# Optimization experiments

Hardware: AMD Instinct MI355X
Metric: run time of the kernel (lower is better)

The kernel has to match this reference:

```python
import jax, jax.numpy as jnp
import numpy as np

HIDDEN = 1024
EMB = HIDDEN // 2          # embedding_dim = hidden_dim // 2
NUM_OPS = 8
BATCH = 16384


def setup_inputs() -> dict:
    key = jax.random.key(0)
    ks = jax.random.split(key, 8)
    x = jax.random.normal(ks[0], (BATCH, HIDDEN), dtype=jnp.float32)
    sampled_ops = jax.random.randint(ks[1], (BATCH,), 0, NUM_OPS, dtype=jnp.int32)
    op_emb = jax.random.normal(ks[2], (NUM_OPS, EMB), dtype=jnp.float32) * 0.02
    # per-expert 2-layer MLP params (Linear stored as [in, out] for x @ W)
    s1 = 1.0 / np.sqrt(HIDDEN + EMB)
    s2 = 1.0 / np.sqrt(HIDDEN)
    W1 = jax.random.uniform(ks[3], (NUM_OPS, HIDDEN + EMB, HIDDEN), jnp.float32, -s1, s1)
    b1 = jax.random.uniform(ks[4], (NUM_OPS, HIDDEN), jnp.float32, -s1, s1)
    W2 = jax.random.uniform(ks[5], (NUM_OPS, HIDDEN, HIDDEN), jnp.float32, -s2, s2)
    b2 = jax.random.uniform(ks[6], (NUM_OPS, HIDDEN), jnp.float32, -s2, s2)
    return {"x": x, "sampled_ops": sampled_ops, "op_emb": op_emb,
            "W1": W1, "b1": b1, "W2": W2, "b2": b2}


def reference(x, sampled_ops, op_emb, W1, b1, W2, b2):
    # gather per-token operator embedding and augment input
    emb = jnp.take(op_emb, sampled_ops, axis=0)            # [B, EMB]
    x_aug = jnp.concatenate([x, emb], axis=-1)             # [B, H+EMB]
    num_ops = W1.shape[0]
    out = jnp.zeros_like(x)
    # loop over the small fixed expert set; mask-combine per token
    for o in range(num_ops):
        h = jax.nn.relu(x_aug @ W1[o] + b1[o])             # [B, H]
        y = jax.nn.relu(h @ W2[o] + b2[o])                 # [B, H]
        mask = (sampled_ops == o)[:, None]
        out = out + jnp.where(mask, y, 0.0)
    return out
```

## Files before the change

kernel.cpp:

```cpp
#include <hip/hip_runtime.h>
#include <hip/hip_bf16.h>

#define BATCH 16384
#define HID   1024
#define EMBD  512
#define NOPS  8
#define MAXT  136
#define CNTS  16

typedef __attribute__((ext_vector_type(8))) short bf16x8;
typedef __attribute__((ext_vector_type(4))) float f32x4;

#define VMWAIT(N) asm volatile("s_waitcnt vmcnt(" #N ")" ::: "memory")
#define BARRIER_FENCED()                      \
  do {                                        \
    asm volatile("" ::: "memory");            \
    __builtin_amdgcn_s_barrier();             \
    asm volatile("" ::: "memory");            \
    __builtin_amdgcn_sched_barrier(0);        \
  } while (0)

__device__ __forceinline__ unsigned short f2bf(float f) {
  unsigned int u = __float_as_uint(f);
  u += 0x7FFF + ((u >> 16) & 1);
  return (unsigned short)(u >> 16);
}

__device__ __forceinline__ unsigned int pk2(float a, float b) {
  __hip_bfloat162 t = __float22bfloat162_rn(make_float2(a, b));
  return *(unsigned int*)(&t);
}

__device__ __forceinline__ void lds_load16(void* lds, const void* g) {
  __builtin_amdgcn_global_load_lds(
      (const __attribute__((address_space(1))) unsigned int*)g,
      (__attribute__((address_space(3))) unsigned int*)lds, 16, 0, 0);
}

__device__ __forceinline__ void decode_bid(int bid, int& g, int& nx) {
  g = 17 * (bid & 7) + (bid >> 6);
  nx = (bid >> 3) & 7;
}

__device__ __forceinline__ int decode_tile(const int* __restrict__ cnt,
                                           int g, int& rs, int& ce_cnt) {
  int e = -1, at = 0;
  rs = 0; ce_cnt = 0;
#pragma unroll
  for (int o = 0; o < NOPS; ++o) {
    int c = cnt[o * CNTS];
    int t = (c + 127) >> 7;
    if (e < 0 && g < at + t) { e = o; rs = (g - at) * 128; ce_cnt = c; }
    at += t;
  }
  return e;
}

__device__ __forceinline__ void w_prep_tile(const float* __restrict__ W,
                                            short* __restrict__ Wp,
                                            int ks, int nx, int tid) {
  int n = tid & 127, kh = tid >> 7;
  const float* src = W + (size_t)(ks * 32 + kh * 16) * 1024 + nx * 128 + n;
  float v[16];
#pragma unroll
  for (int kk = 0; kk < 16; ++kk) v[kk] = src[(size_t)kk * 1024];
  uint4 a, b;
  a.x = pk2(v[0], v[1]);  a.y = pk2(v[2], v[3]);
  a.z = pk2(v[4], v[5]);  a.w = pk2(v[6], v[7]);
  b.x = pk2(v[8], v[9]);  b.y = pk2(v[10], v[11]);
  b.z = pk2(v[12], v[13]); b.w = pk2(v[14], v[15]);
  uint4* dst = (uint4*)Wp;
  dst[(2 * kh) * 128 + n]     = a;
  dst[(2 * kh + 1) * 128 + n] = b;
}

__global__ void bucket_ce_k(const int* __restrict__ ops, int* __restrict__ cnt,
                            int* __restrict__ idx, const float* __restrict__ W1,
                            const float* __restrict__ emb,
                            const float* __restrict__ b1, float* __restrict__ ce,
                            short* __restrict__ W1p, const float* __restrict__ x,
                            unsigned int* __restrict__ xb) {
  int bid = blockIdx.x;
  int tid = threadIdx.x;
  if (bid >= 2240) {
    size_t i = ((size_t)(bid - 2240) * 256 + tid) * 16;
    const float4* src = (const float4*)(x + i);
    float4 f0 = src[0], f1 = src[1], f2v = src[2], f3 = src[3];
    uint4 p0 = make_uint4(pk2(f0.x, f0.y), pk2(f0.z, f0.w),
                          pk2(f1.x, f1.y), pk2(f1.z, f1.w));
    uint4 p1 = make_uint4(pk2(f2v.x, f2v.y), pk2(f2v.z, f2v.w),
                          pk2(f3.x, f3.y), pk2(f3.z, f3.w));
    uint4* dst = (uint4*)(xb + i / 2);
    dst[0] = p0;
    dst[1] = p1;
    return;
  }
  if (bid >= 192) {
    int b = bid - 192;
    int e = b / 256; int rr = b % 256; int nx = rr / 32, ks = rr % 32;
    w_prep_tile(W1 + (size_t)e * 1536 * 1024,
                W1p + ((size_t)(e * 8 + nx) * 32 + ks) * 4096, ks, nx, tid);
    return;
  }
  if (bid >= 64) {
    int cb = bid - 64;
    int e = cb >> 4, kp = cb & 15;
    int n = tid * 4;
    const float* Wc = W1 + (size_t)e * 1536 * 1024 + (size_t)(1024 + kp * 32) * 1024 + n;
    const float* ee = emb + e * EMBD + kp * 32;
    float4 a = make_float4(0.f, 0.f, 0.f, 0.f);
#pragma unroll
    for (int kk = 0; kk < 32; ++kk) {
      float s = ee[kk];
      float4 r = *(const float4*)(Wc + (size_t)kk * 1024);
      a.x += s * r.x; a.y += s * r.y; a.z += s * r.z; a.w += s * r.w;
    }
    if (kp == 0) {
      float4 b = *(const float4*)(b1 + e * HID + n);
      a.x += b.x; a.y += b.y; a.z += b.z; a.w += b.w;
    }
    float* d = ce + e * HID + n;
    atomicAdd(d + 0, a.x); atomicAdd(d + 1, a.y);
    atomicAdd(d + 2, a.z); atomicAdd(d + 3, a.w);
    return;
  }
  __shared__ int wcnt[4][NOPS];
  __shared__ int wbase[4][NOPS];
  int lane = tid & 63, w = tid >> 6;
  int t = bid * 256 + tid;
  int op = ops[t];
  unsigned long long msave = 0;
#pragma unroll
  for (int o = 0; o < NOPS; ++o) {
    unsigned long long mm = __ballot(op == o);
    if (op == o) msave = mm;
    if (lane == o) wcnt[w][o] = __popcll(mm);
  }
  __syncthreads();
  if (tid < NOPS) {
    int c0 = wcnt[0][tid], c1 = wcnt[1][tid], c2 = wcnt[2][tid], c3 = wcnt[3][tid];
    int base = atomicAdd(&cnt[tid * CNTS], c0 + c1 + c2 + c3);
    wbase[0][tid] = base;
    wbase[1][tid] = base + c0;
    wbase[2][tid] = base + c0 + c1;
    wbase[3][tid] = base + c0 + c1 + c2;
  }
  __syncthreads();
  int pre = __popcll(msave & ((1ull << lane) - 1ull));
  idx[op * BATCH + wbase[w][op] + pre] = t;
}

__global__ __launch_bounds__(256, 3) void gemm1_w2_k(
    const unsigned int* __restrict__ xb, const int* __restrict__ idx,
    const float* __restrict__ ce, const short* __restrict__ W1p,
    unsigned short* __restrict__ hp, const int* __restrict__ cnt,
    const float* __restrict__ W2, short* __restrict__ W2p) {
  int bid = blockIdx.x;
  int tid = threadIdx.x;
  if (bid >= 8 * MAXT) {
    int b = bid - 8 * MAXT;
    int e = b / 256; int rr = b % 256; int nx = rr / 32, ks = rr % 32;
    w_prep_tile(W2 + (size_t)e * 1024 * 1024,
                W2p + ((size_t)(e * 8 + nx) * 32 + ks) * 4096, ks, nx, tid);
    return;
  }
  int g, nx;
  decode_bid(bid, g, nx);
  int rs, ce_cnt;
  int e = decode_tile(cnt, g, rs, ce_cnt);
  if (e < 0) return;

  __shared__ __align__(16) char smem[49152];
  char* s0 = smem;
  char* s1 = smem + 16384;
  char* s2 = smem + 32768;

  int lane = tid & 63, w = tid >> 6;
  int wm = w >> 1, wn = w & 1;
  int fr = lane & 15, fq = lane >> 4;

  int r0 = w * 32 + (lane >> 2);
  int r1 = r0 + 16;
  int qs = (lane & 3) ^ ((lane >> 3) & 3);
  int pp0 = rs + r0, pp1 = rs + r1;
  int t0 = (pp0 < ce_cnt) ? idx[e * BATCH + pp0] : 0;
  int t1 = (pp1 < ce_cnt) ? idx[e * BATCH + pp1] : 0;
  const char* pa0 = (const char*)xb + (size_t)t0 * 2048 + qs * 16;
  const char* pa1 = (const char*)xb + (size_t)t1 * 2048 + qs * 16;
  const char* pb0 = (const char*)W1p + (size_t)(e * 8 + nx) * 32 * 8192
                    + w * 1024 + lane * 16;
  const char* pb1 = pb0 + 4096;

#define G1_STAGE(NB)                                                          \
  {                                                                           \
    lds_load16((NB) + w * 2048,         pa0);                                 \
    lds_load16((NB) + w * 2048 + 1024,  pa1);                                 \
    lds_load16((NB) + 8192 + w * 1024,  pb0);                                 \
    lds_load16((NB) + 12288 + w * 1024, pb1);                                 \
    pa0 += 64; pa1 += 64; pb0 += 8192; pb1 += 8192;                           \
  }

#define G1_COMP(CB)                                                           \
  {                                                                           \
    const short* lA_ = (const short*)(CB);                                    \
    const short* lB_ = (const short*)((CB) + 8192);                           \
    bf16x8 af[4], bfr[4];                                                     \
    _Pragma("unroll")                                                         \
    for (int i = 0; i < 4; ++i) af[i] = *(const bf16x8*)&lA_[fo + i * 512];   \
    _Pragma("unroll")                                                         \
    for (int j = 0; j < 4; ++j) bfr[j] = *(const bf16x8*)&lB_[bo + j * 128];  \
    _Pragma("unroll")                                                         \
    for (int i = 0; i < 4; ++i)                                               \
      _Pragma("unroll")                                                       \
      for (int j = 0; j < 4; ++j)                                             \
        acc[i][j] = __builtin_amdgcn_mfma_f32_16x16x32_bf16(af[i], bfr[j],    \
                                                            acc[i][j], 0, 0, 0); \
  }

#define G1_STEP(CB, NB)                                                       \
  {                                                                           \
    G1_STAGE(NB);                                                             \
    G1_COMP(CB);                                                              \
    VMWAIT(4);                                                                \
    BARRIER_FENCED();                                                         \
  }

  G1_STAGE(s0);
  G1_STAGE(s1);
  VMWAIT(4);
  BARRIER_FENCED();

  f32x4 acc[4][4] = {};
  int fo = (wm * 64 + fr) * 32 + (fq ^ ((fr >> 1) & 3)) * 8;
  int bo = (fq * 128 + wn * 64 + fr) * 8;

  for (int it = 0; it < 10; ++it) {
    G1_STEP(s0, s2);
    G1_STEP(s1, s0);
    G1_STEP(s2, s1);
  }
  G1_COMP(s0);
  VMWAIT(0);
  BARRIER_FENCED();
  G1_COMP(s1);

#undef G1_STEP
#undef G1_COMP
#undef G1_STAGE

  float bias[4];
#pragma unroll
  for (int j = 0; j < 4; ++j)
    bias[j] = ce[e * HID + nx * 128 + wn * 64 + j * 16 + fr];

  int lr = lane >> 2;
#pragma unroll
  for (int i = 0; i < 4; ++i) {
    __syncthreads();
#pragma unroll
    for (int j = 0; j < 4; ++j)
#pragma unroll
      for (int rg = 0; rg < 4; ++rg) {
        float v = acc[i][j][rg] + bias[j];
        v = v > 0.f ? v : 0.f;
        int row16 = fq * 4 + rg;
        int off = w * 2048 + row16 * 128 + (j * 16 + fr) * 2;
        off ^= (row16 & 1) << 6;
        *(unsigned short*)(smem + off) = f2bf(v);
      }
    __syncthreads();
    int R = wm * 64 + i * 16 + lr;
#pragma unroll
    for (int s = 0; s < 2; ++s) {
      int ch = (lane & 3) + s * 4;
      int off = w * 2048 + lr * 128 + ch * 16;
      off ^= (lr & 1) << 6;
      uint4 val = *(const uint4*)(smem + off);
      int ks2 = nx * 4 + wn * 2 + (ch >> 2);
      int kq = ch & 3;
      *(uint4*)(hp + (((size_t)(g * 32 + ks2) * 4 + kq) * 128 + R) * 8) = val;
    }
  }
}

__global__ __launch_bounds__(256, 3) void gemm2_k(
    const unsigned short* __restrict__ hp, const float* __restrict__ b2,
    const short* __restrict__ W2p, float* __restrict__ out,
    const int* __restrict__ idx, const int* __restrict__ cnt) {
  int g, nx;
  decode_bid(blockIdx.x, g, nx);
  int rs, ce_cnt;
  int e = decode_tile(cnt, g, rs, ce_cnt);
  if (e < 0) return;

  __shared__ __align__(16) char smem[49152];
  __shared__ int toks[128];
  char* s0 = smem;
  char* s1 = smem + 16384;
  char* s2 = smem + 32768;

  int tid = threadIdx.x, lane = tid & 63, w = tid >> 6;
  int wm = w >> 1, wn = w & 1;
  int fr = lane & 15, fq = lane >> 4;

  if (tid < 128) {
    int p = rs + tid;
    toks[tid] = (p < ce_cnt) ? idx[e * BATCH + p] : 0;
  }

  const char* Asrc = (const char*)hp + (size_t)g * 32 * 8192;
  const char* Bsrc = (const char*)W2p + (size_t)(e * 8 + nx) * 32 * 8192;
  const char* pA0 = Asrc + w * 1024 + lane * 16;
  const char* pA1 = pA0 + 4096;
  const char* pB0 = Bsrc + w * 1024 + lane * 16;
  const char* pB1 = pB0 + 4096;

#define G2_STAGE(NB)                                                          \
  {                                                                           \
    lds_load16((NB) + w * 1024,         pA0);                                 \
    lds_load16((NB) + 4096 + w * 1024,  pA1);                                 \
    lds_load16((NB) + 8192 + w * 1024,  pB0);                                 \
    lds_load16((NB) + 12288 + w * 1024, pB1);                                 \
    pA0 += 8192; pA1 += 8192; pB0 += 8192; pB1 += 8192;                       \
  }

#define G2_COMP(CB)                                                           \
  {                                                                           \
    const short* lA_ = (const short*)(CB);                                    \
    const short* lB_ = (const short*)((CB) + 8192);                           \
    bf16x8 af[4], bfr[4];                                                     \
    _Pragma("unroll")                                                         \
    for (int i = 0; i < 4; ++i) af[i] = *(const bf16x8*)&lA_[fo + i * 128];   \
    _Pragma("unroll")                                                         \
    for (int j = 0; j < 4; ++j) bfr[j] = *(const bf16x8*)&lB_[bo + j * 128];  \
    _Pragma("unroll")                                                         \
    for (int i = 0; i < 4; ++i)                                               \
      _Pragma("unroll")                                                       \
      for (int j = 0; j < 4; ++j)                                             \
        acc[i][j] = __builtin_amdgcn_mfma_f32_16x16x32_bf16(af[i], bfr[j],    \
                                                            acc[i][j], 0, 0, 0); \
  }

#define G2_STEP(CB, NB)                                                       \
  {                                                                           \
    G2_STAGE(NB);                                                             \
    G2_COMP(CB);                                                              \
    VMWAIT(4);                                                                \
    BARRIER_FENCED();                                                         \
  }

  G2_STAGE(s0);
  G2_STAGE(s1);
  VMWAIT(4);
  BARRIER_FENCED();

  f32x4 acc[4][4] = {};
  int fo = (fq * 128 + wm * 64 + fr) * 8;
  int bo = (fq * 128 + wn * 64 + fr) * 8;

  for (int it = 0; it < 10; ++it) {
    G2_STEP(s0, s2);
    G2_STEP(s1, s0);
    G2_STEP(s2, s1);
  }
  G2_COMP(s0);
  VMWAIT(0);
  BARRIER_FENCED();
  G2_COMP(s1);

#undef G2_STEP
#undef G2_COMP
#undef G2_STAGE

  float bias[4];
#pragma unroll
  for (int j = 0; j < 4; ++j)
    bias[j] = b2[e * HID + nx * 128 + wn * 64 + j * 16 + fr];

  int lr = lane >> 2;
#pragma unroll
  for (int i = 0; i < 4; ++i) {
    __syncthreads();
#pragma unroll
    for (int j = 0; j < 4; ++j)
#pragma unroll
      for (int rg = 0; rg < 4; ++rg) {
        float v = acc[i][j][rg] + bias[j];
        int row16 = fq * 4 + rg;
        int off = w * 4096 + row16 * 256 + (j * 16 + fr) * 4;
        off ^= (row16 & 1) << 6;
        *(float*)(smem + off) = v > 0.f ? v : 0.f;
      }
    __syncthreads();
    int R = wm * 64 + i * 16 + lr;
    if (R < ce_cnt - rs) {
      float* orow = out + (size_t)toks[R] * HID + nx * 128 + wn * 64;
#pragma unroll
      for (int s = 0; s < 4; ++s) {
        int ch = (lane & 3) + s * 4;
        int off = w * 4096 + lr * 256 + ch * 16;
        off ^= (lr & 1) << 6;
        *(float4*)(orow + ch * 4) = *(const float4*)(smem + off);
      }
    }
  }
}


extern "C" void kernel_launch(void* const* d_in, const int* in_sizes, int n_in,
                              void* d_out, int out_size, void* d_ws, size_t ws_size,
                              hipStream_t stream) {
  const float* x   = (const float*)d_in[0];
  const int*   ops = (const int*)d_in[1];
  const float* emb = (const float*)d_in[2];
  const float* W1  = (const float*)d_in[3];
  const float* b1  = (const float*)d_in[4];
  const float* W2  = (const float*)d_in[5];
  const float* b2  = (const float*)d_in[6];
  float* out = (float*)d_out;

  char* ws = (char*)d_ws;
  int* cnt  = (int*)(ws + 0);
  float* ce = (float*)(ws + 512);
  int* idx  = (int*)(ws + 36864);
  short* W1p = (short*)(ws + 561152);
  short* W2p = (short*)(ws + 17338368);
  unsigned short* hp = (unsigned short*)(ws + 34115584);
  unsigned int* xb = (unsigned int*)(ws + 69767168);

  hipMemsetAsync(ws, 0, 33280, stream);
  bucket_ce_k<<<2240 + 4096, 256, 0, stream>>>(ops, cnt, idx, W1, emb, b1, ce, W1p, x, xb);
  gemm1_w2_k<<<8 * MAXT + 2048, 256, 0, stream>>>(xb, idx, ce, W1p, hp, cnt, W2, W2p);
  gemm2_k<<<8 * MAXT, 256, 0, stream>>>(hp, b2, W2p, out, idx, cnt);
}
```

Before: 274.4 us.

## Interleave side-work blocks with main blocks in fused prep and GEMM1 launches

Block IDs in the two fused kernels are remapped so every third block does the primary work (bucketing/ce/W1 prep, or GEMM1 tiles) and the other two do the auxiliary conversions (x to bf16, or W2 packing). Previously the auxiliary blocks were appended at the end of the grid and ran only after the main blocks. Interleaving lets memory-bound conversion work run alongside compute-heavy GEMM tiles so the streams of work overlap and tail imbalance shrinks. The grids are padded to multiples of three, so some blocks exit immediately, and the GEMM tile order that was tuned for cache locality is now spread across more hardware slots.

```diff
diff --git a/kernel.cpp b/kernel.cpp
--- a/kernel.cpp
+++ b/kernel.cpp
@@ -37,9 +37,9 @@
       (__attribute__((address_space(3))) unsigned int*)lds, 16, 0, 0);
 }
 
-__device__ __forceinline__ void decode_bid(int bid, int& g, int& nx) {
-  g = 17 * (bid & 7) + (bid >> 6);
-  nx = (bid >> 3) & 7;
+__device__ __forceinline__ void decode_bid(int gb, int& g, int& nx) {
+  g = 17 * (gb & 7) + (gb >> 6);
+  nx = (gb >> 3) & 7;
 }
 
 __device__ __forceinline__ int decode_tile(const int* __restrict__ cnt,
@@ -82,8 +82,11 @@
                             unsigned int* __restrict__ xb) {
   int bid = blockIdx.x;
   int tid = threadIdx.x;
-  if (bid >= 2240) {
-    size_t i = ((size_t)(bid - 2240) * 256 + tid) * 16;
+  int q = bid / 3, r = bid - q * 3;
+  if (r != 0) {
+    int b = 2 * q + (r - 1);
+    if (b >= 4096) return;
+    size_t i = ((size_t)b * 256 + tid) * 16;
     const float4* src = (const float4*)(x + i);
     float4 f0 = src[0], f1 = src[1], f2v = src[2], f3 = src[3];
     uint4 p0 = make_uint4(pk2(f0.x, f0.y), pk2(f0.z, f0.w),
@@ -95,15 +98,15 @@
     dst[1] = p1;
     return;
   }
-  if (bid >= 192) {
-    int b = bid - 192;
+  if (q >= 192) {
+    int b = q - 192;
     int e = b / 256; int rr = b % 256; int nx = rr / 32, ks = rr % 32;
     w_prep_tile(W1 + (size_t)e * 1536 * 1024,
                 W1p + ((size_t)(e * 8 + nx) * 32 + ks) * 4096, ks, nx, tid);
     return;
   }
-  if (bid >= 64) {
-    int cb = bid - 64;
+  if (q >= 64) {
+    int cb = q - 64;
     int e = cb >> 4, kp = cb & 15;
     int n = tid * 4;
     const float* Wc = W1 + (size_t)e * 1536 * 1024 + (size_t)(1024 + kp * 32) * 1024 + n;
@@ -112,8 +115,8 @@
 #pragma unroll
     for (int kk = 0; kk < 32; ++kk) {
       float s = ee[kk];
-      float4 r = *(const float4*)(Wc + (size_t)kk * 1024);
-      a.x += s * r.x; a.y += s * r.y; a.z += s * r.z; a.w += s * r.w;
+      float4 r2 = *(const float4*)(Wc + (size_t)kk * 1024);
+      a.x += s * r2.x; a.y += s * r2.y; a.z += s * r2.z; a.w += s * r2.w;
     }
     if (kp == 0) {
       float4 b = *(const float4*)(b1 + e * HID + n);
@@ -127,7 +130,7 @@
   __shared__ int wcnt[4][NOPS];
   __shared__ int wbase[4][NOPS];
   int lane = tid & 63, w = tid >> 6;
-  int t = bid * 256 + tid;
+  int t = q * 256 + tid;
   int op = ops[t];
   unsigned long long msave = 0;
 #pragma unroll
@@ -157,15 +160,17 @@
     const float* __restrict__ W2, short* __restrict__ W2p) {
   int bid = blockIdx.x;
   int tid = threadIdx.x;
-  if (bid >= 8 * MAXT) {
-    int b = bid - 8 * MAXT;
+  int q = bid / 3, r = bid - q * 3;
+  if (r != 0) {
+    int b = 2 * q + (r - 1);
+    if (b >= 2048) return;
     int e = b / 256; int rr = b % 256; int nx = rr / 32, ks = rr % 32;
     w_prep_tile(W2 + (size_t)e * 1024 * 1024,
                 W2p + ((size_t)(e * 8 + nx) * 32 + ks) * 4096, ks, nx, tid);
     return;
   }
   int g, nx;
-  decode_bid(bid, g, nx);
+  decode_bid(q, g, nx);
   int rs, ce_cnt;
   int e = decode_tile(cnt, g, rs, ce_cnt);
   if (e < 0) return;
@@ -429,7 +434,7 @@
   unsigned int* xb = (unsigned int*)(ws + 69767168);
 
   hipMemsetAsync(ws, 0, 33280, stream);
-  bucket_ce_k<<<2240 + 4096, 256, 0, stream>>>(ops, cnt, idx, W1, emb, b1, ce, W1p, x, xb);
-  gemm1_w2_k<<<8 * MAXT + 2048, 256, 0, stream>>>(xb, idx, ce, W1p, hp, cnt, W2, W2p);
+  bucket_ce_k<<<6720, 256, 0, stream>>>(ops, cnt, idx, W1, emb, b1, ce, W1p, x, xb);
+  gemm1_w2_k<<<3264, 256, 0, stream>>>(xb, idx, ce, W1p, hp, cnt, W2, W2p);
   gemm2_k<<<8 * MAXT, 256, 0, stream>>>(hp, b2, W2p, out, idx, cnt);
 }
```

Result: no change. 278.4 us (+1.5%).

## Widen GEMM1 block tile to 128x256 to reuse A tiles across two N slices

Applied to the files above, without the earlier changes.

Each GEMM1 block now computes two adjacent 128-column output slices instead of one. Each gathered activation tile is loaded once and used for twice as many MFMAs, and the GEMM1 grid is halved. The cost is doubled accumulator registers, a larger LDS footprint of 72KB triple-buffered, and launch bounds lowered from 3 to 2 blocks per CU, so occupancy and latency hiding drop.

```diff
diff --git a/kernel.cpp b/kernel.cpp
--- a/kernel.cpp
+++ b/kernel.cpp
@@ -40,6 +40,11 @@
 __device__ __forceinline__ void decode_bid(int bid, int& g, int& nx) {
   g = 17 * (bid & 7) + (bid >> 6);
   nx = (bid >> 3) & 7;
+}
+
+__device__ __forceinline__ void decode_bid2(int gb, int& g, int& nx2) {
+  g = 17 * (gb & 7) + (gb >> 5);
+  nx2 = (gb >> 3) & 3;
 }
 
 __device__ __forceinline__ int decode_tile(const int* __restrict__ cnt,
@@ -150,30 +155,30 @@
   idx[op * BATCH + wbase[w][op] + pre] = t;
 }
 
-__global__ __launch_bounds__(256, 3) void gemm1_w2_k(
+__global__ __launch_bounds__(256, 2) void gemm1_w2_k(
     const unsigned int* __restrict__ xb, const int* __restrict__ idx,
     const float* __restrict__ ce, const short* __restrict__ W1p,
     unsigned short* __restrict__ hp, const int* __restrict__ cnt,
     const float* __restrict__ W2, short* __restrict__ W2p) {
   int bid = blockIdx.x;
   int tid = threadIdx.x;
-  if (bid >= 8 * MAXT) {
-    int b = bid - 8 * MAXT;
+  if (bid >= 544) {
+    int b = bid - 544;
     int e = b / 256; int rr = b % 256; int nx = rr / 32, ks = rr % 32;
     w_prep_tile(W2 + (size_t)e * 1024 * 1024,
                 W2p + ((size_t)(e * 8 + nx) * 32 + ks) * 4096, ks, nx, tid);
     return;
   }
-  int g, nx;
-  decode_bid(bid, g, nx);
+  int g, nx2;
+  decode_bid2(bid, g, nx2);
   int rs, ce_cnt;
   int e = decode_tile(cnt, g, rs, ce_cnt);
   if (e < 0) return;
 
-  __shared__ __align__(16) char smem[49152];
+  __shared__ __align__(16) char smem[73728];
   char* s0 = smem;
-  char* s1 = smem + 16384;
-  char* s2 = smem + 32768;
+  char* s1 = smem + 24576;
+  char* s2 = smem + 49152;
 
   int lane = tid & 63, w = tid >> 6;
   int wm = w >> 1, wn = w & 1;
@@ -187,50 +192,59 @@
   int t1 = (pp1 < ce_cnt) ? idx[e * BATCH + pp1] : 0;
   const char* pa0 = (const char*)xb + (size_t)t0 * 2048 + qs * 16;
   const char* pa1 = (const char*)xb + (size_t)t1 * 2048 + qs * 16;
-  const char* pb0 = (const char*)W1p + (size_t)(e * 8 + nx) * 32 * 8192
-                    + w * 1024 + lane * 16;
-  const char* pb1 = pb0 + 4096;
+  const char* pb00 = (const char*)W1p + (size_t)(e * 8 + nx2 * 2) * 32 * 8192
+                     + w * 1024 + lane * 16;
+  const char* pb01 = pb00 + 4096;
+  const char* pb10 = pb00 + 262144;
+  const char* pb11 = pb10 + 4096;
 
 #define G1_STAGE(NB)                                                          \
   {                                                                           \
     lds_load16((NB) + w * 2048,         pa0);                                 \
     lds_load16((NB) + w * 2048 + 1024,  pa1);                                 \
-    lds_load16((NB) + 8192 + w * 1024,  pb0);                                 \
-    lds_load16((NB) + 12288 + w * 1024, pb1);                                 \
-    pa0 += 64; pa1 += 64; pb0 += 8192; pb1 += 8192;                           \
+    lds_load16((NB) + 8192 + w * 1024,  pb00);                                \
+    lds_load16((NB) + 12288 + w * 1024, pb01);                                \
+    lds_load16((NB) + 16384 + w * 1024, pb10);                                \
+    lds_load16((NB) + 20480 + w * 1024, pb11);                                \
+    pa0 += 64; pa1 += 64;                                                     \
+    pb00 += 8192; pb01 += 8192; pb10 += 8192; pb11 += 8192;                   \
   }
 
 #define G1_COMP(CB)                                                           \
   {                                                                           \
-    const short* lA_ = (const short*)(CB);                                    \
-    const short* lB_ = (const short*)((CB) + 8192);                           \
-    bf16x8 af[4], bfr[4];                                                     \
+    const short* lA_  = (const short*)(CB);                                   \
+    const short* lB0_ = (const short*)((CB) + 8192);                          \
+    const short* lB1_ = (const short*)((CB) + 16384);                         \
+    bf16x8 af[4], bfr[8];                                                     \
     _Pragma("unroll")                                                         \
     for (int i = 0; i < 4; ++i) af[i] = *(const bf16x8*)&lA_[fo + i * 512];   \
     _Pragma("unroll")                                                         \
-    for (int j = 0; j < 4; ++j) bfr[j] = *(const bf16x8*)&lB_[bo + j * 128];  \
+    for (int j = 0; j < 4; ++j) {                                             \
+      bfr[j]     = *(const bf16x8*)&lB0_[bo + j * 128];                       \
+      bfr[4 + j] = *(const bf16x8*)&lB1_[bo + j * 128];                       \
+    }                                                                         \
     _Pragma("unroll")                                                         \
     for (int i = 0; i < 4; ++i)                                               \
       _Pragma("unroll")                                                       \
-      for (int j = 0; j < 4; ++j)                                             \
-        acc[i][j] = __builtin_amdgcn_mfma_f32_16x16x32_bf16(af[i], bfr[j],    \
-                                                            acc[i][j], 0, 0, 0); \
+      for (int jj = 0; jj < 8; ++jj)                                          \
+        acc[i][jj] = __builtin_amdgcn_mfma_f32_16x16x32_bf16(af[i], bfr[jj],  \
+                                                             acc[i][jj], 0, 0, 0); \
   }
 
 #define G1_STEP(CB, NB)                                                       \
   {                                                                           \
     G1_STAGE(NB);                                                             \
     G1_COMP(CB);                                                              \
-    VMWAIT(4);                                                                \
+    VMWAIT(6);                                                                \
     BARRIER_FENCED();                                                         \
   }
 
   G1_STAGE(s0);
   G1_STAGE(s1);
-  VMWAIT(4);
+  VMWAIT(6);
   BARRIER_FENCED();
 
-  f32x4 acc[4][4] = {};
+  f32x4 acc[4][8] = {};
   int fo = (wm * 64 + fr) * 32 + (fq ^ ((fr >> 1) & 3)) * 8;
   int bo = (fq * 128 + wn * 64 + fr) * 8;
 
@@ -248,37 +262,43 @@
 #undef G1_COMP
 #undef G1_STAGE
 
-  float bias[4];
-#pragma unroll
-  for (int j = 0; j < 4; ++j)
-    bias[j] = ce[e * HID + nx * 128 + wn * 64 + j * 16 + fr];
+  float bias[2][4];
+#pragma unroll
+  for (int h = 0; h < 2; ++h)
+#pragma unroll
+    for (int j = 0; j < 4; ++j)
+      bias[h][j] = ce[e * HID + (nx2 * 2 + h) * 128 + wn * 64 + j * 16 + fr];
 
   int lr = lane >> 2;
 #pragma unroll
-  for (int i = 0; i < 4; ++i) {
-    __syncthreads();
-#pragma unroll
-    for (int j = 0; j < 4; ++j)
-#pragma unroll
-      for (int rg = 0; rg < 4; ++rg) {
-        float v = acc[i][j][rg] + bias[j];
-        v = v > 0.f ? v : 0.f;
-        int row16 = fq * 4 + rg;
-        int off = w * 2048 + row16 * 128 + (j * 16 + fr) * 2;
-        off ^= (row16 & 1) << 6;
-        *(unsigned short*)(smem + off) = f2bf(v);
+  for (int h = 0; h < 2; ++h) {
+    int nx = nx2 * 2 + h;
+#pragma unroll
+    for (int i = 0; i < 4; ++i) {
+      __syncthreads();
+#pragma unroll
+      for (int j = 0; j < 4; ++j)
+#pragma unroll
+        for (int rg = 0; rg < 4; ++rg) {
+          float v = acc[i][h * 4 + j][rg] + bias[h][j];
+          v = v > 0.f ? v : 0.f;
+          int row16 = fq * 4 + rg;
+          int off = w * 2048 + row16 * 128 + (j * 16 + fr) * 2;
+          off ^= (row16 & 1) << 6;
+          *(unsigned short*)(smem + off) = f2bf(v);
+        }
+      __syncthreads();
+      int R = wm * 64 + i * 16 + lr;
+#pragma unroll
+      for (int s = 0; s < 2; ++s) {
+        int ch = (lane & 3) + s * 4;
+        int off = w * 2048 + lr * 128 + ch * 16;
+        off ^= (lr & 1) << 6;
+        uint4 val = *(const uint4*)(smem + off);
+        int ks2 = nx * 4 + wn * 2 + (ch >> 2);
+        int kq = ch & 3;
+        *(uint4*)(hp + (((size_t)(g * 32 + ks2) * 4 + kq) * 128 + R) * 8) = val;
       }
-    __syncthreads();
-    int R = wm * 64 + i * 16 + lr;
-#pragma unroll
-    for (int s = 0; s < 2; ++s) {
-      int ch = (lane & 3) + s * 4;
-      int off = w * 2048 + lr * 128 + ch * 16;
-      off ^= (lr & 1) << 6;
-      uint4 val = *(const uint4*)(smem + off);
-      int ks2 = nx * 4 + wn * 2 + (ch >> 2);
-      int kq = ch & 3;
-      *(uint4*)(hp + (((size_t)(g * 32 + ks2) * 4 + kq) * 128 + R) * 8) = val;
     }
   }
 }
@@ -430,6 +450,6 @@
 
   hipMemsetAsync(ws, 0, 33280, stream);
   bucket_ce_k<<<2240 + 4096, 256, 0, stream>>>(ops, cnt, idx, W1, emb, b1, ce, W1p, x, xb);
-  gemm1_w2_k<<<8 * MAXT + 2048, 256, 0, stream>>>(xb, idx, ce, W1p, hp, cnt, W2, W2p);
+  gemm1_w2_k<<<544 + 2048, 256, 0, stream>>>(xb, idx, ce, W1p, hp, cnt, W2, W2p);
   gemm2_k<<<8 * MAXT, 256, 0, stream>>>(hp, b2, W2p, out, idx, cnt);
 }
```

Measured after the change: 273.3 us. Within noise of the previous version (-0.4%).
